# Performance work log

Hardware: AMD Instinct MI355X
Metric: run time of the kernel (lower is better)

The kernel has to match this reference:

```python
import jax, jax.numpy as jnp
import numpy as np
from jax import lax

H = 1024      # hidden_size
M = 256       # memory_size
NH = 4        # num_heads
HD = M // NH  # head_dim = 64
EPS = 1e-5


def _ln(x, g, b):
    mu = jnp.mean(x, axis=-1, keepdims=True)
    var = jnp.mean(jnp.square(x - mu), axis=-1, keepdims=True)
    return (x - mu) * lax.rsqrt(var + EPS) * g + b


def setup_inputs() -> dict:
    key = jax.random.key(0)
    ks = jax.random.split(key, 12)
    B, S, NM = 8, 2048, 4096
    s = 0.02
    return {
        "query_hidden": jax.random.normal(ks[0], (B, S, H), jnp.float32),
        "mem_keys": jax.random.normal(ks[1], (NM, M), jnp.float32),
        "selection_scores": jax.random.uniform(ks[2], (NM,), jnp.float32),
        "qp_w": jax.random.normal(ks[3], (M, H), jnp.float32) * s,
        "qp_b": jnp.zeros((M,), jnp.float32),
        "in_proj_w": jax.random.normal(ks[4], (3 * M, M), jnp.float32) * s,
        "in_proj_b": jnp.zeros((3 * M,), jnp.float32),
        "out_w": jax.random.normal(ks[5], (M, M), jnp.float32) * s,
        "out_b": jnp.zeros((M,), jnp.float32),
        "gate_w": jax.random.normal(ks[6], (H, H + M), jnp.float32) * s,
        "gate_b": jnp.zeros((H,), jnp.float32),
        "int_w1": jax.random.normal(ks[7], (2 * H, H + M), jnp.float32) * s,
        "int_b1": jnp.zeros((2 * H,), jnp.float32),
        "int_ln_g": jnp.ones((2 * H,), jnp.float32),
        "int_ln_b": jnp.zeros((2 * H,), jnp.float32),
        "int_w2": jax.random.normal(ks[8], (H, 2 * H), jnp.float32) * s,
        "int_b2": jnp.zeros((H,), jnp.float32),
        "ln1_g": jnp.ones((M,), jnp.float32),
        "ln1_b": jnp.zeros((M,), jnp.float32),
        "ln2_g": jnp.ones((H,), jnp.float32),
        "ln2_b": jnp.zeros((H,), jnp.float32),
        "top_k": 512,
    }


def reference(query_hidden, mem_keys, selection_scores, qp_w, qp_b,
              in_proj_w, in_proj_b, out_w, out_b, gate_w, gate_b,
              int_w1, int_b1, int_ln_g, int_ln_b, int_w2, int_b2,
              ln1_g, ln1_b, ln2_g, ln2_b, top_k):
    B, S, _ = query_hidden.shape
    # query projection into memory space: [B,S,M]
    q_emb = query_hidden @ qp_w.T + qp_b
    # top-k memory selection by scores (static k)
    _, idx = lax.top_k(selection_scores, top_k)
    mem = mem_keys[idx]                      # [K, M]
    mem = _ln(mem, ln1_g, ln1_b)
    # MultiheadAttention (batch_first, eval mode). Per-position loop in the
    # original is equivalent to one batched attention (no mask).
    wq, wk, wv = jnp.split(in_proj_w, 3, axis=0)
    bq, bk, bv = jnp.split(in_proj_b, 3, axis=0)
    q = (q_emb @ wq.T + bq).reshape(B, S, NH, HD)
    k = (mem @ wk.T + bk).reshape(-1, NH, HD)   # [K,NH,HD]
    v = (mem @ wv.T + bv).reshape(-1, NH, HD)
    scores = jnp.einsum('bshd,khd->bhsk', q, k) / np.sqrt(HD).astype(jnp.float32)
    attn = jax.nn.softmax(scores, axis=-1)
    ctx = jnp.einsum('bhsk,khd->bshd', attn, v).reshape(B, S, M)
    attn_out = ctx @ out_w.T + out_b            # [B,S,M]
    # gated integration
    cat = jnp.concatenate([query_hidden, attn_out], axis=-1)  # [B,S,H+M]
    gate = jax.nn.sigmoid(cat @ gate_w.T + gate_b)
    h = _ln(cat @ int_w1.T + int_b1, int_ln_g, int_ln_b)
    h = jax.nn.gelu(h, approximate=False)
    integrated = h @ int_w2.T + int_b2
    out = _ln(query_hidden + gate * integrated, ln2_g, ln2_b)
    return out
```

## Files before the change

### kernel.cpp

```cpp
#include <hip/hip_runtime.h>
#include <math.h>


typedef __bf16 bf16x8 __attribute__((ext_vector_type(8)));
typedef __bf16 bf16x4 __attribute__((ext_vector_type(4)));
typedef float  floatx4 __attribute__((ext_vector_type(4)));

#define NMEM   4096
#define KSEL   512

__device__ __forceinline__ void gl_lds16(const __bf16* g, __bf16* l) {
  __builtin_amdgcn_global_load_lds(
      (const __attribute__((address_space(1))) void*)g,
      (__attribute__((address_space(3))) void*)l, 16, 0, 0);
}

__global__ void cvt_kernel(const float* __restrict__ s0, const float* __restrict__ s1,
                           const float* __restrict__ s2, const float* __restrict__ s3,
                           const float* __restrict__ s4,
                           __bf16* __restrict__ d0, __bf16* __restrict__ d1,
                           __bf16* __restrict__ d2, __bf16* __restrict__ d3,
                           __bf16* __restrict__ d4) {
  long q = (long)blockIdx.x * 256 + threadIdx.x;
  const long n0 = 16777216 / 4, n1 = 65536 / 4, n2 = 1310720 / 4,
             n3 = 2621440 / 4, n4 = 2097152 / 4;
  const float* s; __bf16* d; long off;
  if (q < n0) { s = s0; d = d0; off = q; }
  else if ((q -= n0) < n1) { s = s1; d = d1; off = q; }
  else if ((q -= n1) < n2) { s = s2; d = d2; off = q; }
  else if ((q -= n2) < n3) { s = s3; d = d3; off = q; }
  else if ((q -= n3) < n4) { s = s4; d = d4; off = q; }
  else return;
  float4 v = ((const float4*)s)[off];
  bf16x4 o;
  o[0] = (__bf16)v.x; o[1] = (__bf16)v.y; o[2] = (__bf16)v.z; o[3] = (__bf16)v.w;
  ((bf16x4*)d)[off] = o;
}

__device__ __forceinline__ unsigned mapbits(float x) {
  unsigned b = __float_as_uint(x);
  return (b & 0x80000000u) ? ~b : (b | 0x80000000u);
}

__global__ void topk_kernel(const float* __restrict__ scores, int* __restrict__ idx_out) {
  const int n = NMEM, k = KSEL;
  __shared__ int hist[256];
  __shared__ int s_need;
  __shared__ unsigned s_prefix;
  __shared__ int s_cnt_gt, s_ntie;
  __shared__ int tie[1024];
  int tid = threadIdx.x;
  if (tid == 0) { s_need = k; s_prefix = 0; s_cnt_gt = 0; s_ntie = 0; }
  __syncthreads();
  for (int pass = 0; pass < 4; ++pass) {
    if (tid < 256) hist[tid] = 0;
    __syncthreads();
    int shift = 24 - 8 * pass;
    unsigned pref = s_prefix;
    for (int i = tid; i < n; i += 256) {
      unsigned u = mapbits(scores[i]);
      bool in = (pass == 0) || ((u >> (shift + 8)) == pref);
      if (in) atomicAdd(&hist[(u >> shift) & 255], 1);
    }
    __syncthreads();
    if (tid == 0) {
      int need = s_need, above = 0, b = 255;
      for (;; --b) {
        int c = hist[b];
        if (above + c >= need) { s_need = need - above; break; }
        above += c;
      }
      s_prefix = (s_prefix << 8) | (unsigned)b;
    }
    __syncthreads();
  }
  unsigned T = s_prefix;
  int need = s_need;
  for (int i = tid; i < n; i += 256) {
    unsigned u = mapbits(scores[i]);
    if (u > T) { int p = atomicAdd(&s_cnt_gt, 1); idx_out[p] = i; }
    else if (u == T) { int t = atomicAdd(&s_ntie, 1); if (t < 1024) tie[t] = i; }
  }
  __syncthreads();
  int base = s_cnt_gt;
  int nt = s_ntie < 1024 ? s_ntie : 1024;
  for (int j = tid; j < nt; j += 256) {
    int my = tie[j], rank = 0;
    for (int l = 0; l < nt; ++l) rank += (tie[l] < my) ? 1 : 0;
    if (rank < need) idx_out[base + rank] = my;
  }
}

__global__ void wc_build(const float* __restrict__ qp_w, const float* __restrict__ qp_b,
                         const float* __restrict__ in_w, const float* __restrict__ in_b,
                         __bf16* __restrict__ Wc, float* __restrict__ bcq) {
  int i = blockIdx.x, t = threadIdx.x;
  const float* wq = in_w + (long)i * 256;
  float a0 = 0, a1 = 0, a2 = 0, a3 = 0;
  for (int s = 0; s < 256; ++s) {
    float wv = wq[s];
    const float* qr = qp_w + (long)s * 1024 + t;
    a0 += wv * qr[0];   a1 += wv * qr[256];
    a2 += wv * qr[512]; a3 += wv * qr[768];
  }
  __bf16* wr = Wc + (long)i * 1024 + t;
  wr[0]   = (__bf16)(0.125f * a0); wr[256] = (__bf16)(0.125f * a1);
  wr[512] = (__bf16)(0.125f * a2); wr[768] = (__bf16)(0.125f * a3);
  if (t == 0) {
    float s = in_b[i];
    for (int j = 0; j < 256; ++j) s += wq[j] * qp_b[j];
    bcq[i] = 0.125f * s;
  }
}

__global__ void kv_build(const int* __restrict__ idx, const float* __restrict__ mem_keys,
                         const float* __restrict__ in_w, const float* __restrict__ in_b,
                         const float* __restrict__ ln1g, const float* __restrict__ ln1b,
                         __bf16* __restrict__ Kmat, __bf16* __restrict__ Vt) {
  int r = blockIdx.x, t = threadIdx.x;
  int lane = t & 63, wave = t >> 6;
  __shared__ float wred[8];
  __shared__ float m[256];
  int row = idx[r];
  float x = mem_keys[(long)row * 256 + t];
  float s = x;
  #pragma unroll
  for (int o = 32; o > 0; o >>= 1) s += __shfl_xor(s, o);
  if (lane == 0) wred[wave] = s;
  __syncthreads();
  float mu = (wred[0] + wred[1] + wred[2] + wred[3]) / 256.0f;
  float e = x - mu;
  s = e * e;
  #pragma unroll
  for (int o = 32; o > 0; o >>= 1) s += __shfl_xor(s, o);
  if (lane == 0) wred[4 + wave] = s;
  __syncthreads();
  float rstd = rsqrtf((wred[4] + wred[5] + wred[6] + wred[7]) / 256.0f + 1e-5f);
  m[t] = e * rstd * ln1g[t] + ln1b[t];
  __syncthreads();
  float ka = 0.f, va = 0.f;
  const float* wk = in_w + (long)(256 + t) * 256;
  const float* wv = in_w + (long)(512 + t) * 256;
  #pragma unroll 4
  for (int i = 0; i < 256; i += 4) {
    float4 wkv = *(const float4*)(wk + i);
    float4 wvv = *(const float4*)(wv + i);
    ka += m[i] * wkv.x + m[i + 1] * wkv.y + m[i + 2] * wkv.z + m[i + 3] * wkv.w;
    va += m[i] * wvv.x + m[i + 1] * wvv.y + m[i + 2] * wvv.z + m[i + 3] * wvv.w;
  }
  ka += in_b[256 + t]; va += in_b[512 + t];
  Kmat[(long)r * 256 + t] = (__bf16)ka;
  Vt[(long)(t >> 6) * (64 * 512) + (long)(t & 63) * 512 + r] = (__bf16)va;
}

template <int BM, int BN, int EPI>
__launch_bounds__(256, 4)
__global__ void gemm_kernel(const __bf16* __restrict__ X1, int ldx1, int K1,
                            const __bf16* __restrict__ X2, int ldx2,
                            const __bf16* __restrict__ W, int ldw,
                            const float* __restrict__ bias,
                            const __bf16* __restrict__ gmul,
                            __bf16* __restrict__ C, int ldc, int Ktot,
                            long sXz, long sWz, long sCz) {
  constexpr int BK = 64;
  __shared__ __bf16 As[BM * BK];
  __shared__ __bf16 Bs[BN * BK];
  const int tid = threadIdx.x;
  const int lane = tid & 63, wave = tid >> 6;
  const int wm = wave >> 1, wn = wave & 1;
  constexpr int FM = (BM / 2) / 16, FN = (BN / 2) / 16;
  floatx4 acc[FM][FN];
  #pragma unroll
  for (int i = 0; i < FM; ++i)
    #pragma unroll
    for (int j = 0; j < FN; ++j)
      #pragma unroll
      for (int r = 0; r < 4; ++r) acc[i][j][r] = 0.0f;

  const long z = blockIdx.z;
  const __bf16* x1 = X1 + z * sXz;
  const __bf16* w  = W + z * sWz;
  __bf16* c = C + z * sCz;
  const long row0 = (long)blockIdx.x * BM;
  const int col0 = blockIdx.y * BN;
  const int nKt = Ktot / BK;
  const int srow = lane >> 3;
  const int scol = ((lane & 7) ^ srow) * 8;

  for (int kt = 0; kt < nKt; ++kt) {
    const int k0 = kt * BK;
    const __bf16* xb; long xld; int kx;
    if (k0 < K1) { xb = x1; xld = ldx1; kx = k0; }
    else         { xb = X2; xld = ldx2; kx = k0 - K1; }
    #pragma unroll
    for (int i = 0; i < BM / 32; ++i) {
      int chunk = wave * (BM / 32) + i;
      const __bf16* g = xb + (row0 + chunk * 8 + srow) * xld + kx + scol;
      gl_lds16(g, As + chunk * 512);
    }
    #pragma unroll
    for (int i = 0; i < BN / 32; ++i) {
      int chunk = wave * (BN / 32) + i;
      const __bf16* g = w + (long)(col0 + chunk * 8 + srow) * ldw + k0 + scol;
      gl_lds16(g, Bs + chunk * 512);
    }
    __syncthreads();
    #pragma unroll
    for (int kk = 0; kk < 2; ++kk) {
      bf16x8 a[FM], b[FN];
      const int ccq = kk * 4 + (lane >> 4);
      #pragma unroll
      for (int fm = 0; fm < FM; ++fm) {
        const int r = wm * (BM / 2) + fm * 16 + (lane & 15);
        a[fm] = *(const bf16x8*)(As + r * BK + ((ccq ^ (r & 7)) << 3));
      }
      #pragma unroll
      for (int fn = 0; fn < FN; ++fn) {
        const int r = wn * (BN / 2) + fn * 16 + (lane & 15);
        b[fn] = *(const bf16x8*)(Bs + r * BK + ((ccq ^ (r & 7)) << 3));
      }
      #pragma unroll
      for (int fm = 0; fm < FM; ++fm)
        #pragma unroll
        for (int fn = 0; fn < FN; ++fn)
          acc[fm][fn] = __builtin_amdgcn_mfma_f32_16x16x32_bf16(a[fm], b[fn], acc[fm][fn], 0, 0, 0);
    }
    __syncthreads();
  }
  #pragma unroll
  for (int fn = 0; fn < FN; ++fn) {
    const int col = col0 + wn * (BN / 2) + fn * 16 + (lane & 15);
    float bv = (EPI == 1) ? 0.0f : bias[col];
    #pragma unroll
    for (int fm = 0; fm < FM; ++fm) {
      #pragma unroll
      for (int r = 0; r < 4; ++r) {
        long row = row0 + wm * (BM / 2) + fm * 16 + (lane >> 4) * 4 + r;
        float v = acc[fm][fn][r] + bv;
        if (EPI == 2) v = 1.0f / (1.0f + __expf(-v));
        if (EPI == 3) v *= (float)gmul[row * (long)ldc + col];
        c[row * (long)ldc + col] = (__bf16)v;
      }
    }
  }
}

__launch_bounds__(256, 2)
__global__ void flash_kernel(const __bf16* __restrict__ Q, const __bf16* __restrict__ Km,
                             const __bf16* __restrict__ Vt, __bf16* __restrict__ Ctx) {
  __shared__ __bf16 Qs[64 * 64];
  __shared__ __bf16 Ks[128 * 64];
  __shared__ __bf16 Vs[64 * 128];
  __shared__ __bf16 Ps[64 * 128];
  __shared__ float mpart[2][64], spart[2][64];
  __shared__ float m_run[64], l_run[64];
  const int tid = threadIdx.x, lane = tid & 63, wave = tid >> 6;
  const int wm = wave >> 1, wn = wave & 1;
  const long row0 = (long)blockIdx.x * 64;
  const int h = blockIdx.y;
  const int srow = lane >> 3, scc = lane & 7;
  const int q4 = lane >> 4, l15 = lane & 15;

  if (tid < 64) { m_run[tid] = -3e38f; l_run[tid] = 0.f; }
  #pragma unroll
  for (int i = 0; i < 2; ++i) {
    int chunk = wave * 2 + i;
    int r = chunk * 8 + srow;
    gl_lds16(Q + (row0 + r) * 256 + h * 64 + ((scc ^ (r & 7)) << 3), Qs + chunk * 512);
  }
  floatx4 oacc[2][2];
  #pragma unroll
  for (int fm = 0; fm < 2; ++fm)
    #pragma unroll
    for (int fn = 0; fn < 2; ++fn)
      #pragma unroll
      for (int r = 0; r < 4; ++r) oacc[fm][fn][r] = 0.f;

  for (int c = 0; c < 4; ++c) {
    #pragma unroll
    for (int i = 0; i < 4; ++i) {
      int chunk = wave * 4 + i;
      int r = chunk * 8 + srow;
      gl_lds16(Km + (long)(c * 128 + r) * 256 + h * 64 + ((scc ^ (r & 7)) << 3),
               Ks + chunk * 512);
    }
    #pragma unroll
    for (int i = 0; i < 4; ++i) {
      int chunk = wave * 4 + i;
      int d = chunk * 4 + q4;
      int cc = l15 ^ (d & 7);
      gl_lds16(Vt + (long)h * 32768 + (long)d * 512 + c * 128 + cc * 8,
               Vs + chunk * 512);
    }
    __syncthreads();

    floatx4 sacc[2][4];
    #pragma unroll
    for (int fm = 0; fm < 2; ++fm)
      #pragma unroll
      for (int fn = 0; fn < 4; ++fn)
        #pragma unroll
        for (int r = 0; r < 4; ++r) sacc[fm][fn][r] = 0.f;
    #pragma unroll
    for (int kk = 0; kk < 2; ++kk) {
      bf16x8 a[2], b[4];
      const int ccq = kk * 4 + q4;
      #pragma unroll
      for (int fm = 0; fm < 2; ++fm) {
        const int r = wm * 32 + fm * 16 + l15;
        a[fm] = *(const bf16x8*)(Qs + r * 64 + ((ccq ^ (r & 7)) << 3));
      }
      #pragma unroll
      for (int fn = 0; fn < 4; ++fn) {
        const int r = wn * 64 + fn * 16 + l15;
        b[fn] = *(const bf16x8*)(Ks + r * 64 + ((ccq ^ (r & 7)) << 3));
      }
      #pragma unroll
      for (int fm = 0; fm < 2; ++fm)
        #pragma unroll
        for (int fn = 0; fn < 4; ++fn)
          sacc[fm][fn] = __builtin_amdgcn_mfma_f32_16x16x32_bf16(a[fm], b[fn], sacc[fm][fn], 0, 0, 0);
    }
    #pragma unroll
    for (int fm = 0; fm < 2; ++fm) {
      #pragma unroll
      for (int r = 0; r < 4; ++r) {
        float v = sacc[fm][0][r];
        #pragma unroll
        for (int fn = 1; fn < 4; ++fn) v = fmaxf(v, sacc[fm][fn][r]);
        v = fmaxf(v, __shfl_xor(v, 1)); v = fmaxf(v, __shfl_xor(v, 2));
        v = fmaxf(v, __shfl_xor(v, 4)); v = fmaxf(v, __shfl_xor(v, 8));
        if (l15 == 0) mpart[wn][wm * 32 + fm * 16 + q4 * 4 + r] = v;
      }
    }
    __syncthreads();

    float nm[2][4], al[2][4], rs[2][4];
    #pragma unroll
    for (int fm = 0; fm < 2; ++fm)
      #pragma unroll
      for (int r = 0; r < 4; ++r) {
        int row = wm * 32 + fm * 16 + q4 * 4 + r;
        float pm = fmaxf(mpart[0][row], mpart[1][row]);
        float mo = m_run[row];
        float x = fmaxf(mo, pm);
        nm[fm][r] = x;
        al[fm][r] = __expf(mo - x);
        rs[fm][r] = 0.f;
      }
    #pragma unroll
    for (int fm = 0; fm < 2; ++fm)
      #pragma unroll
      for (int fn = 0; fn < 4; ++fn)
        #pragma unroll
        for (int r = 0; r < 4; ++r) {
          float p = __expf(sacc[fm][fn][r] - nm[fm][r]);
          rs[fm][r] += p;
          int row = wm * 32 + fm * 16 + q4 * 4 + r;
          int key = wn * 64 + fn * 16 + l15;
          Ps[row * 128 + (((key >> 3) ^ (row & 7)) << 3) + (key & 7)] = (__bf16)p;
        }
    #pragma unroll
    for (int fm = 0; fm < 2; ++fm)
      #pragma unroll
      for (int r = 0; r < 4; ++r) {
        float v = rs[fm][r];
        v += __shfl_xor(v, 1); v += __shfl_xor(v, 2);
        v += __shfl_xor(v, 4); v += __shfl_xor(v, 8);
        if (l15 == 0) spart[wn][wm * 32 + fm * 16 + q4 * 4 + r] = v;
      }
    __syncthreads();

    #pragma unroll
    for (int fm = 0; fm < 2; ++fm)
      #pragma unroll
      for (int r = 0; r < 4; ++r) {
        int row = wm * 32 + fm * 16 + q4 * 4 + r;
        if (wn == 0 && l15 == 0) {
          m_run[row] = nm[fm][r];
          l_run[row] = l_run[row] * al[fm][r] + spart[0][row] + spart[1][row];
        }
        #pragma unroll
        for (int fn = 0; fn < 2; ++fn) oacc[fm][fn][r] *= al[fm][r];
      }
    #pragma unroll
    for (int step = 0; step < 4; ++step) {
      bf16x8 a[2], b[2];
      const int ccq = step * 4 + q4;
      #pragma unroll
      for (int fm = 0; fm < 2; ++fm) {
        const int r = wm * 32 + fm * 16 + l15;
        a[fm] = *(const bf16x8*)(Ps + r * 128 + ((ccq ^ (r & 7)) << 3));
      }
      #pragma unroll
      for (int fn = 0; fn < 2; ++fn) {
        const int rv = wn * 32 + fn * 16 + l15;
        b[fn] = *(const bf16x8*)(Vs + rv * 128 + ((ccq ^ (rv & 7)) << 3));
      }
      #pragma unroll
      for (int fm = 0; fm < 2; ++fm)
        #pragma unroll
        for (int fn = 0; fn < 2; ++fn)
          oacc[fm][fn] = __builtin_amdgcn_mfma_f32_16x16x32_bf16(a[fm], b[fn], oacc[fm][fn], 0, 0, 0);
    }
    __syncthreads();
  }
  #pragma unroll
  for (int fm = 0; fm < 2; ++fm)
    #pragma unroll
    for (int r = 0; r < 4; ++r) {
      int row = wm * 32 + fm * 16 + q4 * 4 + r;
      float inv = 1.0f / l_run[row];
      #pragma unroll
      for (int fn = 0; fn < 2; ++fn) {
        int col = wn * 32 + fn * 16 + l15;
        Ctx[(row0 + row) * 256 + h * 64 + col] = (__bf16)(oacc[fm][fn][r] * inv);
      }
    }
}

__global__ void ln_gelu_kernel(__bf16* __restrict__ T1, const float* __restrict__ g,
                               const float* __restrict__ b) {
  long row = blockIdx.x; int t = threadIdx.x;
  int lane = t & 63, wave = t >> 6;
  __shared__ float wred[8];
  __bf16* p = T1 + row * 2048 + t * 8;
  bf16x8 v = *(const bf16x8*)p;
  float f[8], s = 0.f;
  #pragma unroll
  for (int j = 0; j < 8; ++j) { f[j] = (float)v[j]; s += f[j]; }
  #pragma unroll
  for (int o = 32; o > 0; o >>= 1) s += __shfl_xor(s, o);
  if (lane == 0) wred[wave] = s;
  __syncthreads();
  float mu = (wred[0] + wred[1] + wred[2] + wred[3]) / 2048.0f;
  s = 0.f;
  #pragma unroll
  for (int j = 0; j < 8; ++j) { f[j] -= mu; s += f[j] * f[j]; }
  #pragma unroll
  for (int o = 32; o > 0; o >>= 1) s += __shfl_xor(s, o);
  if (lane == 0) wred[4 + wave] = s;
  __syncthreads();
  float rstd = rsqrtf((wred[4] + wred[5] + wred[6] + wred[7]) / 2048.0f + 1e-5f);
  float4 g0 = *(const float4*)(g + t * 8), g1 = *(const float4*)(g + t * 8 + 4);
  float4 b0 = *(const float4*)(b + t * 8), b1 = *(const float4*)(b + t * 8 + 4);
  float gg[8] = { g0.x, g0.y, g0.z, g0.w, g1.x, g1.y, g1.z, g1.w };
  float bb[8] = { b0.x, b0.y, b0.z, b0.w, b1.x, b1.y, b1.z, b1.w };
  bf16x8 o8;
  #pragma unroll
  for (int j = 0; j < 8; ++j) {
    float y = f[j] * rstd * gg[j] + bb[j];
    float u = 1.5957691216057308f * (y + 0.044715f * y * y * y);
    o8[j] = (__bf16)(y / (1.0f + __expf(-u)));
  }
  *(bf16x8*)p = o8;
}

__global__ void final_kernel(const float* __restrict__ qh, const __bf16* __restrict__ gi,
                             const float* __restrict__ g, const float* __restrict__ b,
                             float* __restrict__ out) {
  long row = blockIdx.x; int t = threadIdx.x;
  int lane = t & 63, wave = t >> 6;
  __shared__ float wred[8];
  long base = row * 1024 + t * 4;
  float4 q = *(const float4*)(qh + base);
  bf16x4 gv = *(const bf16x4*)(gi + base);
  float f[4] = { q.x + (float)gv[0], q.y + (float)gv[1],
                 q.z + (float)gv[2], q.w + (float)gv[3] };
  float s = f[0] + f[1] + f[2] + f[3];
  #pragma unroll
  for (int o = 32; o > 0; o >>= 1) s += __shfl_xor(s, o);
  if (lane == 0) wred[wave] = s;
  __syncthreads();
  float mu = (wred[0] + wred[1] + wred[2] + wred[3]) / 1024.0f;
  s = 0.f;
  #pragma unroll
  for (int j = 0; j < 4; ++j) { f[j] -= mu; s += f[j] * f[j]; }
  #pragma unroll
  for (int o = 32; o > 0; o >>= 1) s += __shfl_xor(s, o);
  if (lane == 0) wred[4 + wave] = s;
  __syncthreads();
  float rstd = rsqrtf((wred[4] + wred[5] + wred[6] + wred[7]) / 1024.0f + 1e-5f);
  float4 gv4 = *(const float4*)(g + t * 4);
  float4 bv4 = *(const float4*)(b + t * 4);
  float4 ov;
  ov.x = f[0] * rstd * gv4.x + bv4.x;
  ov.y = f[1] * rstd * gv4.y + bv4.y;
  ov.z = f[2] * rstd * gv4.z + bv4.z;
  ov.w = f[3] * rstd * gv4.w + bv4.w;
  *(float4*)(out + base) = ov;
}

extern "C" void kernel_launch(void* const* d_in, const int* in_sizes, int n_in,
                              void* d_out, int out_size, void* d_ws, size_t ws_size,
                              hipStream_t stream) {
  const float* qh   = (const float*)d_in[0];
  const float* memk = (const float*)d_in[1];
  const float* sel  = (const float*)d_in[2];
  const float* qp_w = (const float*)d_in[3];
  const float* qp_b = (const float*)d_in[4];
  const float* inw  = (const float*)d_in[5];
  const float* inb  = (const float*)d_in[6];
  const float* outw = (const float*)d_in[7];
  const float* outb = (const float*)d_in[8];
  const float* gw   = (const float*)d_in[9];
  const float* gb   = (const float*)d_in[10];
  const float* w1   = (const float*)d_in[11];
  const float* b1   = (const float*)d_in[12];
  const float* lng  = (const float*)d_in[13];
  const float* lnb  = (const float*)d_in[14];
  const float* w2   = (const float*)d_in[15];
  const float* b2   = (const float*)d_in[16];
  const float* ln1g = (const float*)d_in[17];
  const float* ln1b = (const float*)d_in[18];
  const float* ln2g = (const float*)d_in[19];
  const float* ln2b = (const float*)d_in[20];
  float* out = (float*)d_out;
  char* ws = (char*)d_ws;

  const size_t IDX_O   = 0;
  const size_t BCQ_O   = 2048;
  const size_t WCB_O   = 3072;
  const size_t KMAT_O  = 527360;
  const size_t VT_O    = 789504;
  const size_t OUTWB_O = 1051648;
  const size_t GATEW_O = 1182720;
  const size_t INTW1_O = 3804160;
  const size_t INTW2_O = 9047040;
  const size_t QHB_O   = 13241344;
  const size_t QB_O    = 46795776;
  const size_t SB_O    = 55184384;
  const size_t CTX_O   = 122293248;
  const size_t ATTN_O  = 130681856;
  const size_t GATE_O  = 139070464;

  int*    idxb   = (int*)(ws + IDX_O);
  float*  bcq    = (float*)(ws + BCQ_O);
  __bf16* wcb    = (__bf16*)(ws + WCB_O);
  __bf16* kmat   = (__bf16*)(ws + KMAT_O);
  __bf16* vt     = (__bf16*)(ws + VT_O);
  __bf16* outwb  = (__bf16*)(ws + OUTWB_O);
  __bf16* gatewb = (__bf16*)(ws + GATEW_O);
  __bf16* intw1b = (__bf16*)(ws + INTW1_O);
  __bf16* intw2b = (__bf16*)(ws + INTW2_O);
  __bf16* qhb    = (__bf16*)(ws + QHB_O);
  __bf16* gib    = (__bf16*)(ws + QHB_O);
  __bf16* qb     = (__bf16*)(ws + QB_O);
  __bf16* t1b    = (__bf16*)(ws + SB_O);
  __bf16* ctxb   = (__bf16*)(ws + CTX_O);
  __bf16* attnb  = (__bf16*)(ws + ATTN_O);
  __bf16* gateb  = (__bf16*)(ws + GATE_O);
  const __bf16* nullb = nullptr;

  cvt_kernel<<<22336, 256, 0, stream>>>(qh, outw, gw, w1, w2,
                                        qhb, outwb, gatewb, intw1b, intw2b);
  topk_kernel<<<1, 256, 0, stream>>>(sel, idxb);
  wc_build<<<256, 256, 0, stream>>>(qp_w, qp_b, inw, inb, wcb, bcq);
  kv_build<<<512, 256, 0, stream>>>(idxb, memk, inw, inb, ln1g, ln1b, kmat, vt);
  gemm_kernel<64, 128, 0><<<dim3(256, 2, 1), 256, 0, stream>>>(
      qhb, 1024, 1024, nullb, 0, wcb, 1024, bcq, nullb, qb, 256, 1024, 0, 0, 0);
  flash_kernel<<<dim3(256, 4, 1), 256, 0, stream>>>(qb, kmat, vt, ctxb);
  gemm_kernel<64, 128, 0><<<dim3(256, 2, 1), 256, 0, stream>>>(
      ctxb, 256, 256, nullb, 0, outwb, 256, outb, nullb, attnb, 256, 256, 0, 0, 0);
  gemm_kernel<128, 128, 2><<<dim3(128, 8, 1), 256, 0, stream>>>(
      qhb, 1024, 1024, attnb, 256, gatewb, 1280, gb, nullb, gateb, 1024, 1280, 0, 0, 0);
  gemm_kernel<128, 128, 0><<<dim3(128, 16, 1), 256, 0, stream>>>(
      qhb, 1024, 1024, attnb, 256, intw1b, 1280, b1, nullb, t1b, 2048, 1280, 0, 0, 0);
  ln_gelu_kernel<<<16384, 256, 0, stream>>>(t1b, lng, lnb);
  gemm_kernel<128, 128, 3><<<dim3(128, 8, 1), 256, 0, stream>>>(
      t1b, 2048, 2048, nullb, 0, intw2b, 2048, b2, gateb, gib, 1024, 2048, 0, 0, 0);
  final_kernel<<<16384, 256, 0, stream>>>(qh, gib, ln2g, ln2b, out);
}
```

Before: 643.6 us.

## Fuse prep kernels, Q projection into attention, and gate/intermediate GEMMs

Merges the bf16 conversion, Wc build and top-k kernels into one launch. The flash attention kernel now computes the projected query tile itself from the bf16 hidden states and the combined weight Wc, which removes the separate Q GEMM and its intermediate buffer. The gate and int_w1 GEMMs become one GEMM over the contiguous concatenated weights, with a split epilogue that applies sigmoid to the first 1024 columns. A grouped block-index swizzle is added to improve L2 reuse. In exchange, each head recomputes its Q slice, so the hidden-state reads inside attention are repeated four times.

```diff
diff --git a/kernel.cpp b/kernel.cpp
--- a/kernel.cpp
+++ b/kernel.cpp
@@ -8,6 +8,7 @@
 
 #define NMEM   4096
 #define KSEL   512
+#define NCVT   22336
 
 __device__ __forceinline__ void gl_lds16(const __bf16* g, __bf16* l) {
   __builtin_amdgcn_global_load_lds(
@@ -15,45 +16,70 @@
       (__attribute__((address_space(3))) void*)l, 16, 0, 0);
 }
 
-__global__ void cvt_kernel(const float* __restrict__ s0, const float* __restrict__ s1,
-                           const float* __restrict__ s2, const float* __restrict__ s3,
-                           const float* __restrict__ s4,
-                           __bf16* __restrict__ d0, __bf16* __restrict__ d1,
-                           __bf16* __restrict__ d2, __bf16* __restrict__ d3,
-                           __bf16* __restrict__ d4) {
-  long q = (long)blockIdx.x * 256 + threadIdx.x;
-  const long n0 = 16777216 / 4, n1 = 65536 / 4, n2 = 1310720 / 4,
-             n3 = 2621440 / 4, n4 = 2097152 / 4;
-  const float* s; __bf16* d; long off;
-  if (q < n0) { s = s0; d = d0; off = q; }
-  else if ((q -= n0) < n1) { s = s1; d = d1; off = q; }
-  else if ((q -= n1) < n2) { s = s2; d = d2; off = q; }
-  else if ((q -= n2) < n3) { s = s3; d = d3; off = q; }
-  else if ((q -= n3) < n4) { s = s4; d = d4; off = q; }
-  else return;
-  float4 v = ((const float4*)s)[off];
-  bf16x4 o;
-  o[0] = (__bf16)v.x; o[1] = (__bf16)v.y; o[2] = (__bf16)v.z; o[3] = (__bf16)v.w;
-  ((bf16x4*)d)[off] = o;
-}
-
 __device__ __forceinline__ unsigned mapbits(float x) {
   unsigned b = __float_as_uint(x);
   return (b & 0x80000000u) ? ~b : (b | 0x80000000u);
 }
 
-__global__ void topk_kernel(const float* __restrict__ scores, int* __restrict__ idx_out) {
-  const int n = NMEM, k = KSEL;
+__global__ void prep_kernel(const float* __restrict__ s0, const float* __restrict__ s1,
+                            const float* __restrict__ s2, const float* __restrict__ s3,
+                            const float* __restrict__ s4,
+                            __bf16* __restrict__ d0, __bf16* __restrict__ d1,
+                            __bf16* __restrict__ d2, __bf16* __restrict__ d3,
+                            __bf16* __restrict__ d4,
+                            const float* __restrict__ qp_w, const float* __restrict__ qp_b,
+                            const float* __restrict__ in_w, const float* __restrict__ in_b,
+                            __bf16* __restrict__ Wc, float* __restrict__ bcq,
+                            const float* __restrict__ scores, int* __restrict__ idx_out) {
   __shared__ int hist[256];
   __shared__ int s_need;
   __shared__ unsigned s_prefix;
   __shared__ int s_cnt_gt, s_ntie;
   __shared__ int tie[1024];
-  int tid = threadIdx.x;
+  const int bx = blockIdx.x, tid = threadIdx.x;
+
+  if (bx < NCVT) {
+    long q = (long)bx * 256 + tid;
+    const long n0 = 16777216 / 4, n1 = 65536 / 4, n2 = 1310720 / 4,
+               n3 = 2621440 / 4, n4 = 2097152 / 4;
+    const float* s; __bf16* d; long off;
+    if (q < n0) { s = s0; d = d0; off = q; }
+    else if ((q -= n0) < n1) { s = s1; d = d1; off = q; }
+    else if ((q -= n1) < n2) { s = s2; d = d2; off = q; }
+    else if ((q -= n2) < n3) { s = s3; d = d3; off = q; }
+    else if ((q -= n3) < n4) { s = s4; d = d4; off = q; }
+    else return;
+    float4 v = ((const float4*)s)[off];
+    bf16x4 o;
+    o[0] = (__bf16)v.x; o[1] = (__bf16)v.y; o[2] = (__bf16)v.z; o[3] = (__bf16)v.w;
+    ((bf16x4*)d)[off] = o;
+    return;
+  }
+  if (bx < NCVT + 256) {
+    int i = bx - NCVT, t = tid;
+    const float* wq = in_w + (long)i * 256;
+    float a0 = 0, a1 = 0, a2 = 0, a3 = 0;
+    for (int s = 0; s < 256; ++s) {
+      float wv = wq[s];
+      const float* qr = qp_w + (long)s * 1024 + t;
+      a0 += wv * qr[0];   a1 += wv * qr[256];
+      a2 += wv * qr[512]; a3 += wv * qr[768];
+    }
+    __bf16* wr = Wc + (long)i * 1024 + t;
+    wr[0]   = (__bf16)(0.125f * a0); wr[256] = (__bf16)(0.125f * a1);
+    wr[512] = (__bf16)(0.125f * a2); wr[768] = (__bf16)(0.125f * a3);
+    if (t == 0) {
+      float s = in_b[i];
+      for (int j = 0; j < 256; ++j) s += wq[j] * qp_b[j];
+      bcq[i] = 0.125f * s;
+    }
+    return;
+  }
+  const int n = NMEM, k = KSEL;
   if (tid == 0) { s_need = k; s_prefix = 0; s_cnt_gt = 0; s_ntie = 0; }
   __syncthreads();
   for (int pass = 0; pass < 4; ++pass) {
-    if (tid < 256) hist[tid] = 0;
+    hist[tid] = 0;
     __syncthreads();
     int shift = 24 - 8 * pass;
     unsigned pref = s_prefix;
@@ -88,28 +114,6 @@
     int my = tie[j], rank = 0;
     for (int l = 0; l < nt; ++l) rank += (tie[l] < my) ? 1 : 0;
     if (rank < need) idx_out[base + rank] = my;
-  }
-}
-
-__global__ void wc_build(const float* __restrict__ qp_w, const float* __restrict__ qp_b,
-                         const float* __restrict__ in_w, const float* __restrict__ in_b,
-                         __bf16* __restrict__ Wc, float* __restrict__ bcq) {
-  int i = blockIdx.x, t = threadIdx.x;
-  const float* wq = in_w + (long)i * 256;
-  float a0 = 0, a1 = 0, a2 = 0, a3 = 0;
-  for (int s = 0; s < 256; ++s) {
-    float wv = wq[s];
-    const float* qr = qp_w + (long)s * 1024 + t;
-    a0 += wv * qr[0];   a1 += wv * qr[256];
-    a2 += wv * qr[512]; a3 += wv * qr[768];
-  }
-  __bf16* wr = Wc + (long)i * 1024 + t;
-  wr[0]   = (__bf16)(0.125f * a0); wr[256] = (__bf16)(0.125f * a1);
-  wr[512] = (__bf16)(0.125f * a2); wr[768] = (__bf16)(0.125f * a3);
-  if (t == 0) {
-    float s = in_b[i];
-    for (int j = 0; j < 256; ++j) s += wq[j] * qp_b[j];
-    bcq[i] = 0.125f * s;
   }
 }
 
@@ -153,14 +157,17 @@
   Vt[(long)(t >> 6) * (64 * 512) + (long)(t & 63) * 512 + r] = (__bf16)va;
 }
 
-template <int BM, int BN, int EPI>
+template <int BM, int BN, int EPI, bool SWIZ>
 __launch_bounds__(256, 4)
 __global__ void gemm_kernel(const __bf16* __restrict__ X1, int ldx1, int K1,
                             const __bf16* __restrict__ X2, int ldx2,
                             const __bf16* __restrict__ W, int ldw,
                             const float* __restrict__ bias,
+                            const float* __restrict__ bias2,
                             const __bf16* __restrict__ gmul,
-                            __bf16* __restrict__ C, int ldc, int Ktot,
+                            __bf16* __restrict__ C, int ldc,
+                            __bf16* __restrict__ C2, int ldc2,
+                            int Ktot, int nY,
                             long sXz, long sWz, long sCz) {
   constexpr int BK = 64;
   __shared__ __bf16 As[BM * BK];
@@ -177,12 +184,20 @@
       #pragma unroll
       for (int r = 0; r < 4; ++r) acc[i][j][r] = 0.0f;
 
+  int bx, by;
+  if (SWIZ) {
+    int lin = blockIdx.x;
+    int sx = lin & 7, rest = lin >> 3;
+    by = rest % nY; bx = (rest / nY) * 8 + sx;
+  } else {
+    bx = blockIdx.x; by = blockIdx.y;
+  }
   const long z = blockIdx.z;
   const __bf16* x1 = X1 + z * sXz;
   const __bf16* w  = W + z * sWz;
   __bf16* c = C + z * sCz;
-  const long row0 = (long)blockIdx.x * BM;
-  const int col0 = blockIdx.y * BN;
+  const long row0 = (long)bx * BM;
+  const int col0 = by * BN;
   const int nKt = Ktot / BK;
   const int srow = lane >> 3;
   const int scol = ((lane & 7) ^ srow) * 8;
@@ -230,24 +245,37 @@
   #pragma unroll
   for (int fn = 0; fn < FN; ++fn) {
     const int col = col0 + wn * (BN / 2) + fn * 16 + (lane & 15);
-    float bv = (EPI == 1) ? 0.0f : bias[col];
+    float bv;
+    if (EPI == 1) bv = 0.0f;
+    else if (EPI == 4) bv = (col < 1024) ? bias[col] : bias2[col - 1024];
+    else bv = bias[col];
     #pragma unroll
     for (int fm = 0; fm < FM; ++fm) {
       #pragma unroll
       for (int r = 0; r < 4; ++r) {
         long row = row0 + wm * (BM / 2) + fm * 16 + (lane >> 4) * 4 + r;
         float v = acc[fm][fn][r] + bv;
-        if (EPI == 2) v = 1.0f / (1.0f + __expf(-v));
         if (EPI == 3) v *= (float)gmul[row * (long)ldc + col];
-        c[row * (long)ldc + col] = (__bf16)v;
+        if (EPI == 4) {
+          if (col < 1024) {
+            v = 1.0f / (1.0f + __expf(-v));
+            C[row * (long)ldc + col] = (__bf16)v;
+          } else {
+            C2[row * (long)ldc2 + (col - 1024)] = (__bf16)v;
+          }
+        } else {
+          c[row * (long)ldc + col] = (__bf16)v;
+        }
       }
     }
   }
 }
 
 __launch_bounds__(256, 2)
-__global__ void flash_kernel(const __bf16* __restrict__ Q, const __bf16* __restrict__ Km,
-                             const __bf16* __restrict__ Vt, __bf16* __restrict__ Ctx) {
+__global__ void flash_kernel(const __bf16* __restrict__ qh, const __bf16* __restrict__ Wc,
+                             const float* __restrict__ bcq,
+                             const __bf16* __restrict__ Km, const __bf16* __restrict__ Vt,
+                             __bf16* __restrict__ Ctx) {
   __shared__ __bf16 Qs[64 * 64];
   __shared__ __bf16 Ks[128 * 64];
   __shared__ __bf16 Vs[64 * 128];
@@ -262,12 +290,64 @@
   const int q4 = lane >> 4, l15 = lane & 15;
 
   if (tid < 64) { m_run[tid] = -3e38f; l_run[tid] = 0.f; }
-  #pragma unroll
-  for (int i = 0; i < 2; ++i) {
-    int chunk = wave * 2 + i;
-    int r = chunk * 8 + srow;
-    gl_lds16(Q + (row0 + r) * 256 + h * 64 + ((scc ^ (r & 7)) << 3), Qs + chunk * 512);
-  }
+
+  floatx4 qacc[2][2];
+  #pragma unroll
+  for (int fm = 0; fm < 2; ++fm)
+    #pragma unroll
+    for (int fn = 0; fn < 2; ++fn)
+      #pragma unroll
+      for (int r = 0; r < 4; ++r) qacc[fm][fn][r] = 0.f;
+  for (int kt = 0; kt < 8; ++kt) {
+    #pragma unroll
+    for (int jh = 0; jh < 2; ++jh) {
+      #pragma unroll
+      for (int i = 0; i < 2; ++i) {
+        int chunk = wave * 2 + i;
+        int r = chunk * 8 + srow;
+        int kg = kt * 128 + jh * 64 + ((scc ^ (r & 7)) << 3);
+        gl_lds16(qh + (row0 + r) * 1024 + kg, Ks + jh * 4096 + chunk * 512);
+        gl_lds16(Wc + (long)(h * 64 + r) * 1024 + kg, Vs + jh * 4096 + chunk * 512);
+      }
+    }
+    __syncthreads();
+    #pragma unroll
+    for (int jh = 0; jh < 2; ++jh)
+      #pragma unroll
+      for (int kk = 0; kk < 2; ++kk) {
+        bf16x8 a[2], b[2];
+        const int ccq = kk * 4 + q4;
+        #pragma unroll
+        for (int fm = 0; fm < 2; ++fm) {
+          const int r = wm * 32 + fm * 16 + l15;
+          a[fm] = *(const bf16x8*)(Ks + jh * 4096 + r * 64 + ((ccq ^ (r & 7)) << 3));
+        }
+        #pragma unroll
+        for (int fn = 0; fn < 2; ++fn) {
+          const int r = wn * 32 + fn * 16 + l15;
+          b[fn] = *(const bf16x8*)(Vs + jh * 4096 + r * 64 + ((ccq ^ (r & 7)) << 3));
+        }
+        #pragma unroll
+        for (int fm = 0; fm < 2; ++fm)
+          #pragma unroll
+          for (int fn = 0; fn < 2; ++fn)
+            qacc[fm][fn] = __builtin_amdgcn_mfma_f32_16x16x32_bf16(a[fm], b[fn], qacc[fm][fn], 0, 0, 0);
+      }
+    __syncthreads();
+  }
+  #pragma unroll
+  for (int fm = 0; fm < 2; ++fm)
+    #pragma unroll
+    for (int fn = 0; fn < 2; ++fn)
+      #pragma unroll
+      for (int r = 0; r < 4; ++r) {
+        int row = wm * 32 + fm * 16 + q4 * 4 + r;
+        int col = wn * 32 + fn * 16 + l15;
+        float v = qacc[fm][fn][r] + bcq[h * 64 + col];
+        Qs[row * 64 + (((col >> 3) ^ (row & 7)) << 3) + (col & 7)] = (__bf16)v;
+      }
+  __syncthreads();
+
   floatx4 oacc[2][2];
   #pragma unroll
   for (int fm = 0; fm < 2; ++fm)
@@ -528,7 +608,6 @@
   const size_t INTW1_O = 3804160;
   const size_t INTW2_O = 9047040;
   const size_t QHB_O   = 13241344;
-  const size_t QB_O    = 46795776;
   const size_t SB_O    = 55184384;
   const size_t CTX_O   = 122293248;
   const size_t ATTN_O  = 130681856;
@@ -545,29 +624,27 @@
   __bf16* intw2b = (__bf16*)(ws + INTW2_O);
   __bf16* qhb    = (__bf16*)(ws + QHB_O);
   __bf16* gib    = (__bf16*)(ws + QHB_O);
-  __bf16* qb     = (__bf16*)(ws + QB_O);
   __bf16* t1b    = (__bf16*)(ws + SB_O);
   __bf16* ctxb   = (__bf16*)(ws + CTX_O);
   __bf16* attnb  = (__bf16*)(ws + ATTN_O);
   __bf16* gateb  = (__bf16*)(ws + GATE_O);
-  const __bf16* nullb = nullptr;
-
-  cvt_kernel<<<22336, 256, 0, stream>>>(qh, outw, gw, w1, w2,
-                                        qhb, outwb, gatewb, intw1b, intw2b);
-  topk_kernel<<<1, 256, 0, stream>>>(sel, idxb);
-  wc_build<<<256, 256, 0, stream>>>(qp_w, qp_b, inw, inb, wcb, bcq);
+  __bf16* nullb  = nullptr;
+  const float* nullf = nullptr;
+
+  prep_kernel<<<NCVT + 257, 256, 0, stream>>>(
+      qh, outw, gw, w1, w2, qhb, outwb, gatewb, intw1b, intw2b,
+      qp_w, qp_b, inw, inb, wcb, bcq, sel, idxb);
   kv_build<<<512, 256, 0, stream>>>(idxb, memk, inw, inb, ln1g, ln1b, kmat, vt);
-  gemm_kernel<64, 128, 0><<<dim3(256, 2, 1), 256, 0, stream>>>(
-      qhb, 1024, 1024, nullb, 0, wcb, 1024, bcq, nullb, qb, 256, 1024, 0, 0, 0);
-  flash_kernel<<<dim3(256, 4, 1), 256, 0, stream>>>(qb, kmat, vt, ctxb);
-  gemm_kernel<64, 128, 0><<<dim3(256, 2, 1), 256, 0, stream>>>(
-      ctxb, 256, 256, nullb, 0, outwb, 256, outb, nullb, attnb, 256, 256, 0, 0, 0);
-  gemm_kernel<128, 128, 2><<<dim3(128, 8, 1), 256, 0, stream>>>(
-      qhb, 1024, 1024, attnb, 256, gatewb, 1280, gb, nullb, gateb, 1024, 1280, 0, 0, 0);
-  gemm_kernel<128, 128, 0><<<dim3(128, 16, 1), 256, 0, stream>>>(
-      qhb, 1024, 1024, attnb, 256, intw1b, 1280, b1, nullb, t1b, 2048, 1280, 0, 0, 0);
+  flash_kernel<<<dim3(256, 4, 1), 256, 0, stream>>>(qhb, wcb, bcq, kmat, vt, ctxb);
+  gemm_kernel<64, 128, 0, false><<<dim3(256, 2, 1), 256, 0, stream>>>(
+      ctxb, 256, 256, nullb, 0, outwb, 256, outb, nullf, nullb,
+      attnb, 256, nullb, 0, 256, 2, 0, 0, 0);
+  gemm_kernel<128, 128, 4, true><<<dim3(128 * 24, 1, 1), 256, 0, stream>>>(
+      qhb, 1024, 1024, attnb, 256, gatewb, 1280, gb, b1, nullb,
+      gateb, 1024, t1b, 2048, 1280, 24, 0, 0, 0);
   ln_gelu_kernel<<<16384, 256, 0, stream>>>(t1b, lng, lnb);
-  gemm_kernel<128, 128, 3><<<dim3(128, 8, 1), 256, 0, stream>>>(
-      t1b, 2048, 2048, nullb, 0, intw2b, 2048, b2, gateb, gib, 1024, 2048, 0, 0, 0);
+  gemm_kernel<128, 128, 3, true><<<dim3(128 * 8, 1, 1), 256, 0, stream>>>(
+      t1b, 2048, 2048, nullb, 0, intw2b, 2048, b2, nullf, gateb,
+      gib, 1024, nullb, 0, 2048, 8, 0, 0, 0);
   final_kernel<<<16384, 256, 0, stream>>>(qh, gib, ln2g, ln2b, out);
 }
```

New measurement: 600.4 us. 1.07x faster.
